# Kernel optimization log

Hardware: AMD Instinct MI355X
Metric: run time of the kernel (lower is better)

## Reference

```python
import jax, jax.numpy as jnp
import numpy as np

N_HEADS = 16

def setup_inputs() -> dict:
    key = jax.random.key(0)
    ks = jax.random.split(key, 5)
    D = 2048
    x = jax.random.normal(ks[0], (2, 2048, D), dtype=jnp.float32)
    scale = 1.0 / np.sqrt(D)
    Wq = jax.random.normal(ks[1], (D, D), dtype=jnp.float32) * scale
    Wk = jax.random.normal(ks[2], (D, D), dtype=jnp.float32) * scale
    Wv = jax.random.normal(ks[3], (D, D), dtype=jnp.float32) * scale
    Wo = jax.random.normal(ks[4], (D, D), dtype=jnp.float32) * scale
    return {"x": x, "Wq": Wq, "Wk": Wk, "Wv": Wv, "Wo": Wo}


def reference(x, Wq, Wk, Wv, Wo):
    # Causal multi-head attention. The original module computes it one query
    # position at a time (recompute loop) but the math is standard causal MHA:
    # query pos attends to key positions 0..pos.
    B, S, D = x.shape
    H = N_HEADS
    hd = D // H
    def split_heads(t):
        return t.reshape(B, S, H, hd).transpose(0, 2, 1, 3)  # (B,H,S,hd)
    q = split_heads(x @ Wq.T)
    k = split_heads(x @ Wk.T)
    v = split_heads(x @ Wv.T)
    scores = jnp.einsum('bhqd,bhkd->bhqk', q, k) / jnp.sqrt(jnp.asarray(hd, x.dtype))
    causal = jnp.tril(jnp.ones((S, S), dtype=bool))  # (S,S), True where allowed
    scores = jnp.where(causal[None, None], scores, jnp.asarray(-jnp.inf, scores.dtype))
    attn = jax.nn.softmax(scores, axis=-1)
    out = jnp.einsum('bhqk,bhkd->bhqd', attn, v)
    out = out.transpose(0, 2, 1, 3).reshape(B, S, D)
    return out @ Wo.T
```

## Files before the change

### kernel.cpp

```cpp
#include <hip/hip_runtime.h>
#include <stdint.h>

#define DD 2048
#define SS 2048
#define NB 2
#define NH 16
#define HDIM 128
#define MM (NB*SS)

typedef __attribute__((ext_vector_type(8))) short bf16x8;
typedef __attribute__((ext_vector_type(4))) float f32x4;
typedef __attribute__((ext_vector_type(4))) ushort u16x4;

__device__ __forceinline__ float fast_exp2(float x) {
  return __builtin_amdgcn_exp2f(x);
}

__device__ __forceinline__ ushort f2bf(float f) {
  union { float f; uint32_t u; } v; v.f = f;
  uint32_t u = v.u;
  return (ushort)((u + 0x7fffu + ((u >> 16) & 1u)) >> 16);
}

__device__ __forceinline__ void gld_lds16(const ushort* g, ushort* l) {
  __builtin_amdgcn_global_load_lds(
      (const __attribute__((address_space(1))) void*)g,
      (__attribute__((address_space(3))) void*)l, 16, 0, 0);
}

__global__ __launch_bounds__(256) void cvt_all(
    const float* __restrict__ x, const float* __restrict__ wq,
    const float* __restrict__ wk, const float* __restrict__ wv,
    const float* __restrict__ wo, ushort* __restrict__ dst)
{
  int i8 = blockIdx.x * 256 + threadIdx.x;
  const int X8 = MM * DD / 8;
  const int W8 = DD * DD / 8;
  const float* src; int off;
  if (i8 < X8)            { src = x;  off = i8; }
  else if (i8 < X8 +   W8){ src = wq; off = i8 - X8; }
  else if (i8 < X8 + 2*W8){ src = wk; off = i8 - (X8 +   W8); }
  else if (i8 < X8 + 3*W8){ src = wv; off = i8 - (X8 + 2*W8); }
  else                    { src = wo; off = i8 - (X8 + 3*W8); }
  const float4* p = (const float4*)src;
  float4 a = p[(long)off*2], b = p[(long)off*2 + 1];
  bf16x8 o;
  o[0]=(short)f2bf(a.x); o[1]=(short)f2bf(a.y); o[2]=(short)f2bf(a.z); o[3]=(short)f2bf(a.w);
  o[4]=(short)f2bf(b.x); o[5]=(short)f2bf(b.y); o[6]=(short)f2bf(b.z); o[7]=(short)f2bf(b.w);
  *(bf16x8*)(dst + (long)i8*8) = o;
}

template<int MODE>
__global__ __launch_bounds__(256, 2) void gemm_tri(
    const ushort* __restrict__ A, const ushort* __restrict__ Bt,
    ushort* __restrict__ Qo, ushort* __restrict__ Ko, ushort* __restrict__ Vt,
    float* __restrict__ Cf)
{
  __shared__ ushort lds[3 * 12288];
  const int t = threadIdx.x;
  const int bid = blockIdx.x;
  const int xcd = bid & 7, local = bid >> 3;
  const int NBX = (MODE == 0) ? 6 : 2;
  const int bm = local / NBX;
  const int bn = xcd * NBX + (local - bm * NBX);
  const int lane = t & 63, w = t >> 6;
  const int wr = w >> 1, wcn = w & 1;
  const int lr = lane & 15, lg = lane >> 4;

  int aoff[4], boff[2];
#pragma unroll
  for (int i = 0; i < 4; ++i) {
    int p = i*256 + t, ln = p >> 3, sr = (p & 7) ^ (ln & 7);
    aoff[i] = (2*ln + (sr >> 2)) * DD + (sr & 3) * 8;
  }
#pragma unroll
  for (int i = 0; i < 2; ++i) {
    int p = i*256 + t, ln = p >> 3, sr = (p & 7) ^ (ln & 7);
    boff[i] = (2*ln + (sr >> 2)) * DD + (sr & 3) * 8;
  }
  const ushort* Ab = A  + (long)(bm*256) * DD;
  const ushort* Bb = Bt + (long)(bn*128) * DD;

#define STG_A01(KT, BUF) do { const ushort* g_ = Ab + (KT)*32;             \
    ushort* l_ = lds + (BUF)*12288;                                        \
    gld_lds16(g_ + aoff[0], l_ + t*8);                                     \
    gld_lds16(g_ + aoff[1], l_ + (256 + t)*8); } while (0)
#define STG_A23(KT, BUF) do { const ushort* g_ = Ab + (KT)*32;             \
    ushort* l_ = lds + (BUF)*12288;                                        \
    gld_lds16(g_ + aoff[2], l_ + (512 + t)*8);                             \
    gld_lds16(g_ + aoff[3], l_ + (768 + t)*8); } while (0)
#define STG_B(KT, BUF)   do { const ushort* g_ = Bb + (KT)*32;             \
    ushort* l_ = lds + (BUF)*12288 + 8192;                                 \
    gld_lds16(g_ + boff[0], l_ + t*8);                                     \
    gld_lds16(g_ + boff[1], l_ + (256 + t)*8); } while (0)
#define LDA(dst, m) { int r_ = wr*128 + (m)*16 + lr; int ln_ = r_ >> 1;    \
    int sl_ = (lg + ((r_ & 1) << 2)) ^ (ln_ & 7);                          \
    (dst) = *(const bf16x8*)(cb + ln_*128 + sl_*16); }
#define LDB(dst, n) { int r_ = wcn*64 + (n)*16 + lr; int ln_ = r_ >> 1;    \
    int sl_ = (lg + ((r_ & 1) << 2)) ^ (ln_ & 7);                          \
    (dst) = *(const bf16x8*)(cb + 16384 + ln_*128 + sl_*16); }
#define MFMA42(AV, BV, MB, NB_) do {                                       \
    __builtin_amdgcn_s_setprio(1);                                         \
    _Pragma("unroll") for (int m = 0; m < 4; ++m)                          \
    _Pragma("unroll") for (int n = 0; n < 2; ++n)                          \
      acc[(MB)+m][(NB_)+n] = __builtin_amdgcn_mfma_f32_16x16x32_bf16(      \
          AV[m], BV[n], acc[(MB)+m][(NB_)+n], 0, 0, 0);                    \
    __builtin_amdgcn_s_setprio(0); } while (0)
#define SB  __builtin_amdgcn_sched_barrier(0)
#define BAR __builtin_amdgcn_s_barrier()
#define LGKM0 asm volatile("s_waitcnt lgkmcnt(0)" ::: "memory")

  f32x4 acc[8][4] = {};
  const int T = DD / 32;

  STG_A01(0, 0); STG_A23(0, 0); STG_B(0, 0);
  STG_A01(1, 1); STG_A23(1, 1); STG_B(1, 1);
  asm volatile("s_waitcnt vmcnt(6)" ::: "memory");
  SB; BAR; SB;

  for (int kt = 0; kt < T; ++kt) {
    const char* cb = (const char*)lds + (kt % 3) * 24576;
    const int bs = (kt + 2) % 3;
    const bool st = (kt + 2 < T);
    bf16x8 a03[4], a47[4], b01[2], b23[2];
    LDA(a03[0],0); LDA(a03[1],1); LDA(a03[2],2); LDA(a03[3],3);
    LDB(b01[0],0); LDB(b01[1],1);
    if (st) STG_A01(kt+2, bs);
    SB; BAR; LGKM0; SB;
    MFMA42(a03, b01, 0, 0);
    SB; BAR; SB;
    LDA(a47[0],4); LDA(a47[1],5); LDA(a47[2],6); LDA(a47[3],7);
    if (st) STG_A23(kt+2, bs);
    SB; BAR; LGKM0; SB;
    MFMA42(a47, b01, 4, 0);
    SB; BAR; SB;
    LDB(b23[0],2); LDB(b23[1],3);
    if (st) STG_B(kt+2, bs);
    SB; BAR; LGKM0; SB;
    MFMA42(a03, b23, 0, 2);
    SB; BAR; SB;
    if (st)              { asm volatile("s_waitcnt vmcnt(6)" ::: "memory"); }
    else if (kt + 1 < T) { asm volatile("s_waitcnt vmcnt(0)" ::: "memory"); }
    SB; BAR; SB;
    MFMA42(a47, b23, 4, 2);
    SB; BAR; SB;
  }
#undef STG_A01
#undef STG_A23
#undef STG_B
#undef LDA
#undef LDB
#undef MFMA42
#undef SB
#undef BAR
#undef LGKM0

  const int crb = bm*256 + wr*128 + lg*4;
  if (MODE == 0) {
    const int region = bn >> 4;
    const int ccb = (bn & 15)*128 + wcn*64 + lr;
    if (region < 2) {
      const float scale = (region == 0) ? (0.08838834764831845f * 1.4426950408889634f) : 1.0f;
      ushort* C = (region == 0) ? Qo : Ko;
#pragma unroll
      for (int m = 0; m < 8; ++m)
#pragma unroll
        for (int n = 0; n < 4; ++n)
#pragma unroll
          for (int j = 0; j < 4; ++j)
            C[(long)(crb + m*16 + j) * DD + (ccb + n*16)] = f2bf(acc[m][n][j] * scale);
    } else {
#pragma unroll
      for (int m = 0; m < 8; ++m) {
        int sg = crb + m*16;
        int b2 = sg >> 11, s2 = sg & 2047;
#pragma unroll
        for (int n = 0; n < 4; ++n) {
          int colv = ccb + n*16;
          int h2 = colv >> 7, d2 = colv & 127;
          u16x4 pk;
          pk[0] = f2bf(acc[m][n][0]); pk[1] = f2bf(acc[m][n][1]);
          pk[2] = f2bf(acc[m][n][2]); pk[3] = f2bf(acc[m][n][3]);
          *(u16x4*)(Vt + ((long)((b2*NH + h2)*HDIM + d2)) * SS + s2) = pk;
        }
      }
    }
  } else {
    const int ccb = bn*128 + wcn*64 + lr;
#pragma unroll
    for (int m = 0; m < 8; ++m)
#pragma unroll
      for (int n = 0; n < 4; ++n)
#pragma unroll
        for (int j = 0; j < 4; ++j)
          Cf[(long)(crb + m*16 + j) * DD + (ccb + n*16)] = acc[m][n][j];
  }
}

__global__ __launch_bounds__(512, 4) void attn_fwd(
    const ushort* __restrict__ Qb, const ushort* __restrict__ Kb,
    const ushort* __restrict__ Vtg, ushort* __restrict__ Ob)
{
  __shared__ ushort Ks[64*128];
  __shared__ ushort Vs[128*64];
  __shared__ ushort Ps[8*16*72];

  const int bid = blockIdx.x;
  const int qt = 15 - (bid >> 5);
  const int bh = bid & 31;
  const int b = bh >> 4, h = bh & 15;
  const int t = threadIdx.x;
  const int lane = t & 63;
  const int wq = t >> 6;
  const int lr = lane & 15, lg = lane >> 4;

  const int qbase = qt * 128;
  const long rowQ = (long)(b * SS + qbase + wq * 16);

  bf16x8 qf[4];
#pragma unroll
  for (int c = 0; c < 4; ++c)
    qf[c] = *(const bf16x8*)(Qb + (rowQ + lr) * DD + h*HDIM + c*32 + lg*8);

  f32x4 accO[8] = {};
  float mrow[4], lrow[4];
#pragma unroll
  for (int j = 0; j < 4; ++j) { mrow[j] = -1e30f; lrow[j] = 0.f; }

  const ushort* Kgb = Kb + (long)(b * SS) * DD + h * HDIM;
  const int kr0 = t >> 4, kr1 = 32 + (t >> 4), kci = t & 15;
  const ushort* gk0 = Kgb + (long)kr0 * DD + (kci ^ (kr0 & 7)) * 8;
  const ushort* gk1 = Kgb + (long)kr1 * DD + (kci ^ (kr1 & 7)) * 8;
  ushort* lk0 = Ks + t*8;
  ushort* lk1 = Ks + 4096 + t*8;

  const ushort* Vgb = Vtg + (long)(bh * HDIM) * SS;
  const int vd0 = t >> 3, vd1 = 64 + (t >> 3), vci = t & 7;
  const ushort* gv0 = Vgb + (long)vd0 * SS + (vci ^ (vd0 & 7)) * 8;
  const ushort* gv1 = Vgb + (long)vd1 * SS + (vci ^ (vd1 & 7)) * 8;
  ushort* lv0 = Vs + t*8;
  ushort* lv1 = Vs + 4096 + t*8;

  const int ktmax = 2*qt + 1;
  const int qminw = qbase + wq*16;
  const int qmaxw = qminw + 15;
  ushort* myP = Ps + wq * (16*72);

  for (int kt = 0; kt <= ktmax; ++kt) {
    const int k0 = kt * 64;
    gld_lds16(gk0, lk0); gld_lds16(gk1, lk1);
    gld_lds16(gv0, lv0); gld_lds16(gv1, lv1);
    gk0 += (long)64 * DD; gk1 += (long)64 * DD;
    gv0 += 64; gv1 += 64;
    __syncthreads();

    if (k0 <= qmaxw) {
      f32x4 sc[4] = {};
#pragma unroll
      for (int n = 0; n < 4; ++n) {
        int r = n*16 + lr;
        int swz = (r & 7) << 4;
#pragma unroll
        for (int c = 0; c < 4; ++c) {
          bf16x8 kf = *(const bf16x8*)((const char*)Ks + ((r*256 + c*64 + lg*16) ^ swz));
          sc[n] = __builtin_amdgcn_mfma_f32_16x16x32_bf16(qf[c], kf, sc[n], 0,0,0);
        }
      }
      if (k0 + 63 > qminw) {
#pragma unroll
        for (int n = 0; n < 4; ++n)
#pragma unroll
          for (int j = 0; j < 4; ++j) {
            int kpos = k0 + n*16 + lr;
            int qpos = qminw + lg*4 + j;
            if (kpos > qpos) sc[n][j] = -1e30f;
          }
      }
      float al[4];
#pragma unroll
      for (int j = 0; j < 4; ++j) {
        float tm = fmaxf(fmaxf(sc[0][j], sc[1][j]), fmaxf(sc[2][j], sc[3][j]));
#pragma unroll
        for (int off = 1; off < 16; off <<= 1) tm = fmaxf(tm, __shfl_xor(tm, off));
        float mn = fmaxf(mrow[j], tm);
        float a = fast_exp2(mrow[j] - mn);
        mrow[j] = mn;
        float ts = 0.f;
#pragma unroll
        for (int n = 0; n < 4; ++n) {
          float p = fast_exp2(sc[n][j] - mn);
          sc[n][j] = p; ts += p;
        }
#pragma unroll
        for (int off = 1; off < 16; off <<= 1) ts += __shfl_xor(ts, off);
        lrow[j] = lrow[j] * a + ts;
        al[j] = a;
      }
#pragma unroll
      for (int dg = 0; dg < 8; ++dg) {
        f32x4 v = accO[dg];
        v[0] *= al[0]; v[1] *= al[1]; v[2] *= al[2]; v[3] *= al[3];
        accO[dg] = v;
      }
#pragma unroll
      for (int n = 0; n < 4; ++n)
#pragma unroll
        for (int j = 0; j < 4; ++j)
          myP[(lg*4 + j)*72 + n*16 + lr] = f2bf(sc[n][j]);
      bf16x8 pa0 = *(const bf16x8*)(myP + lr*72 + lg*8);
      bf16x8 pa1 = *(const bf16x8*)(myP + lr*72 + 32 + lg*8);
#pragma unroll
      for (int dg = 0; dg < 8; ++dg) {
        int d = dg*16 + lr;
        int vswz = (d & 7) << 4;
        bf16x8 v0 = *(const bf16x8*)((const char*)Vs + ((d*128 + lg*16) ^ vswz));
        bf16x8 v1 = *(const bf16x8*)((const char*)Vs + ((d*128 + 64 + lg*16) ^ vswz));
        accO[dg] = __builtin_amdgcn_mfma_f32_16x16x32_bf16(pa0, v0, accO[dg], 0,0,0);
        accO[dg] = __builtin_amdgcn_mfma_f32_16x16x32_bf16(pa1, v1, accO[dg], 0,0,0);
      }
    }
    __syncthreads();
  }

  float inv[4];
#pragma unroll
  for (int j = 0; j < 4; ++j) inv[j] = 1.0f / lrow[j];
  ushort* Og = Ob + rowQ * DD + h * HDIM;
#pragma unroll
  for (int dg = 0; dg < 8; ++dg)
#pragma unroll
    for (int j = 0; j < 4; ++j)
      Og[(long)(lg*4 + j) * DD + dg*16 + lr] = f2bf(accO[dg][j] * inv[j]);
}

extern "C" void kernel_launch(void* const* d_in, const int* in_sizes, int n_in,
                              void* d_out, int out_size, void* d_ws, size_t ws_size,
                              hipStream_t stream) {
  const float* x  = (const float*)d_in[0];
  const float* Wq = (const float*)d_in[1];
  const float* Wk = (const float*)d_in[2];
  const float* Wv = (const float*)d_in[3];
  const float* Wo = (const float*)d_in[4];

  ushort* ws  = (ushort*)d_ws;
  ushort* xb  = ws;
  ushort* wqb = ws  + (long)MM*DD;
  ushort* wkb = wqb + (long)DD*DD;
  ushort* wvb = wkb + (long)DD*DD;
  ushort* wob = wvb + (long)DD*DD;
  ushort* Qb  = wob + (long)DD*DD;
  ushort* Kb  = Qb  + (long)MM*DD;
  ushort* Vtg = Kb  + (long)MM*DD;
  (void)wkb; (void)wvb;

  const int CVT_BLOCKS = (MM*DD + 4*DD*DD) / 8 / 256;
  cvt_all<<<CVT_BLOCKS, 256, 0, stream>>>(x, Wq, Wk, Wv, Wo, ws);

  gemm_tri<0><<<768, 256, 0, stream>>>(xb, wqb, Qb, Kb, Vtg, nullptr);

  attn_fwd<<<512, 512, 0, stream>>>(Qb, Kb, Vtg, xb);

  gemm_tri<1><<<256, 256, 0, stream>>>(xb, wob, nullptr, nullptr, nullptr,
                                       (float*)d_out);
}
```

Baseline: 274.8 us.

## Process 32 query rows per wave in attention to reuse K/V fragments

```diff
diff --git a/kernel.cpp b/kernel.cpp
--- a/kernel.cpp
+++ b/kernel.cpp
@@ -197,13 +197,13 @@
   }
 }
 
-__global__ __launch_bounds__(512, 4) void attn_fwd(
+__global__ __launch_bounds__(256, 3) void attn_fwd(
     const ushort* __restrict__ Qb, const ushort* __restrict__ Kb,
     const ushort* __restrict__ Vtg, ushort* __restrict__ Ob)
 {
   __shared__ ushort Ks[64*128];
   __shared__ ushort Vs[128*64];
-  __shared__ ushort Ps[8*16*72];
+  __shared__ ushort Ps[4*32*68];
 
   const int bid = blockIdx.x;
   const int qt = 15 - (bid >> 5);
@@ -215,47 +215,54 @@
   const int lr = lane & 15, lg = lane >> 4;
 
   const int qbase = qt * 128;
-  const long rowQ = (long)(b * SS + qbase + wq * 16);
-
-  bf16x8 qf[4];
-#pragma unroll
-  for (int c = 0; c < 4; ++c)
-    qf[c] = *(const bf16x8*)(Qb + (rowQ + lr) * DD + h*HDIM + c*32 + lg*8);
-
-  f32x4 accO[8] = {};
-  float mrow[4], lrow[4];
-#pragma unroll
-  for (int j = 0; j < 4; ++j) { mrow[j] = -1e30f; lrow[j] = 0.f; }
+  const long rowQ = (long)(b * SS + qbase + wq * 32);
+
+  bf16x8 qf[2][4];
+#pragma unroll
+  for (int i = 0; i < 2; ++i)
+#pragma unroll
+    for (int c = 0; c < 4; ++c)
+      qf[i][c] = *(const bf16x8*)(Qb + (rowQ + i*16 + lr) * DD + h*HDIM + c*32 + lg*8);
+
+  f32x4 accO[2][8] = {};
+  float mrow[2][4], lrow[2][4];
+#pragma unroll
+  for (int i = 0; i < 2; ++i)
+#pragma unroll
+    for (int j = 0; j < 4; ++j) { mrow[i][j] = -1e30f; lrow[i][j] = 0.f; }
 
   const ushort* Kgb = Kb + (long)(b * SS) * DD + h * HDIM;
-  const int kr0 = t >> 4, kr1 = 32 + (t >> 4), kci = t & 15;
-  const ushort* gk0 = Kgb + (long)kr0 * DD + (kci ^ (kr0 & 7)) * 8;
-  const ushort* gk1 = Kgb + (long)kr1 * DD + (kci ^ (kr1 & 7)) * 8;
-  ushort* lk0 = Ks + t*8;
-  ushort* lk1 = Ks + 4096 + t*8;
-
+  const ushort* gk[4]; ushort* lk[4];
+#pragma unroll
+  for (int i = 0; i < 4; ++i) {
+    int c = i*256 + t, kr = c >> 4, kc = c & 15;
+    gk[i] = Kgb + (long)kr * DD + (kc ^ (kr & 7)) * 8;
+    lk[i] = Ks + c*8;
+  }
   const ushort* Vgb = Vtg + (long)(bh * HDIM) * SS;
-  const int vd0 = t >> 3, vd1 = 64 + (t >> 3), vci = t & 7;
-  const ushort* gv0 = Vgb + (long)vd0 * SS + (vci ^ (vd0 & 7)) * 8;
-  const ushort* gv1 = Vgb + (long)vd1 * SS + (vci ^ (vd1 & 7)) * 8;
-  ushort* lv0 = Vs + t*8;
-  ushort* lv1 = Vs + 4096 + t*8;
+  const ushort* gv[4]; ushort* lv[4];
+#pragma unroll
+  for (int i = 0; i < 4; ++i) {
+    int c = i*256 + t, vd = c >> 3, vc = c & 7;
+    gv[i] = Vgb + (long)vd * SS + (vc ^ (vd & 7)) * 8;
+    lv[i] = Vs + c*8;
+  }
 
   const int ktmax = 2*qt + 1;
-  const int qminw = qbase + wq*16;
-  const int qmaxw = qminw + 15;
-  ushort* myP = Ps + wq * (16*72);
+  const int qminw = qbase + wq*32;
+  const int qmaxw = qminw + 31;
+  ushort* myP = Ps + wq * (32*68);
 
   for (int kt = 0; kt <= ktmax; ++kt) {
     const int k0 = kt * 64;
-    gld_lds16(gk0, lk0); gld_lds16(gk1, lk1);
-    gld_lds16(gv0, lv0); gld_lds16(gv1, lv1);
-    gk0 += (long)64 * DD; gk1 += (long)64 * DD;
-    gv0 += 64; gv1 += 64;
+#pragma unroll
+    for (int i = 0; i < 4; ++i) { gld_lds16(gk[i], lk[i]); gk[i] += (long)64 * DD; }
+#pragma unroll
+    for (int i = 0; i < 4; ++i) { gld_lds16(gv[i], lv[i]); gv[i] += 64; }
     __syncthreads();
 
     if (k0 <= qmaxw) {
-      f32x4 sc[4] = {};
+      f32x4 sc[2][4] = {};
 #pragma unroll
       for (int n = 0; n < 4; ++n) {
         int r = n*16 + lr;
@@ -263,74 +270,92 @@
 #pragma unroll
         for (int c = 0; c < 4; ++c) {
           bf16x8 kf = *(const bf16x8*)((const char*)Ks + ((r*256 + c*64 + lg*16) ^ swz));
-          sc[n] = __builtin_amdgcn_mfma_f32_16x16x32_bf16(qf[c], kf, sc[n], 0,0,0);
+          sc[0][n] = __builtin_amdgcn_mfma_f32_16x16x32_bf16(qf[0][c], kf, sc[0][n], 0,0,0);
+          sc[1][n] = __builtin_amdgcn_mfma_f32_16x16x32_bf16(qf[1][c], kf, sc[1][n], 0,0,0);
         }
       }
       if (k0 + 63 > qminw) {
 #pragma unroll
+        for (int i = 0; i < 2; ++i)
+#pragma unroll
+          for (int n = 0; n < 4; ++n)
+#pragma unroll
+            for (int j = 0; j < 4; ++j) {
+              int kpos = k0 + n*16 + lr;
+              int qpos = qminw + i*16 + lg*4 + j;
+              if (kpos > qpos) sc[i][n][j] = -1e30f;
+            }
+      }
+      float al[2][4];
+#pragma unroll
+      for (int i = 0; i < 2; ++i)
+#pragma unroll
+        for (int j = 0; j < 4; ++j) {
+          float tm = fmaxf(fmaxf(sc[i][0][j], sc[i][1][j]), fmaxf(sc[i][2][j], sc[i][3][j]));
+#pragma unroll
+          for (int off = 1; off < 16; off <<= 1) tm = fmaxf(tm, __shfl_xor(tm, off));
+          float mn = fmaxf(mrow[i][j], tm);
+          float a = fast_exp2(mrow[i][j] - mn);
+          mrow[i][j] = mn;
+          float ts = 0.f;
+#pragma unroll
+          for (int n = 0; n < 4; ++n) {
+            float p = fast_exp2(sc[i][n][j] - mn);
+            sc[i][n][j] = p; ts += p;
+          }
+#pragma unroll
+          for (int off = 1; off < 16; off <<= 1) ts += __shfl_xor(ts, off);
+          lrow[i][j] = lrow[i][j] * a + ts;
+          al[i][j] = a;
+        }
+#pragma unroll
+      for (int i = 0; i < 2; ++i)
+#pragma unroll
+        for (int dg = 0; dg < 8; ++dg) {
+          f32x4 v = accO[i][dg];
+          v[0] *= al[i][0]; v[1] *= al[i][1]; v[2] *= al[i][2]; v[3] *= al[i][3];
+          accO[i][dg] = v;
+        }
+#pragma unroll
+      for (int i = 0; i < 2; ++i)
+#pragma unroll
         for (int n = 0; n < 4; ++n)
 #pragma unroll
-          for (int j = 0; j < 4; ++j) {
-            int kpos = k0 + n*16 + lr;
-            int qpos = qminw + lg*4 + j;
-            if (kpos > qpos) sc[n][j] = -1e30f;
-          }
-      }
-      float al[4];
-#pragma unroll
-      for (int j = 0; j < 4; ++j) {
-        float tm = fmaxf(fmaxf(sc[0][j], sc[1][j]), fmaxf(sc[2][j], sc[3][j]));
-#pragma unroll
-        for (int off = 1; off < 16; off <<= 1) tm = fmaxf(tm, __shfl_xor(tm, off));
-        float mn = fmaxf(mrow[j], tm);
-        float a = fast_exp2(mrow[j] - mn);
-        mrow[j] = mn;
-        float ts = 0.f;
-#pragma unroll
-        for (int n = 0; n < 4; ++n) {
-          float p = fast_exp2(sc[n][j] - mn);
-          sc[n][j] = p; ts += p;
-        }
-#pragma unroll
-        for (int off = 1; off < 16; off <<= 1) ts += __shfl_xor(ts, off);
-        lrow[j] = lrow[j] * a + ts;
-        al[j] = a;
-      }
-#pragma unroll
-      for (int dg = 0; dg < 8; ++dg) {
-        f32x4 v = accO[dg];
-        v[0] *= al[0]; v[1] *= al[1]; v[2] *= al[2]; v[3] *= al[3];
-        accO[dg] = v;
-      }
-#pragma unroll
-      for (int n = 0; n < 4; ++n)
-#pragma unroll
-        for (int j = 0; j < 4; ++j)
-          myP[(lg*4 + j)*72 + n*16 + lr] = f2bf(sc[n][j]);
-      bf16x8 pa0 = *(const bf16x8*)(myP + lr*72 + lg*8);
-      bf16x8 pa1 = *(const bf16x8*)(myP + lr*72 + 32 + lg*8);
+          for (int j = 0; j < 4; ++j)
+            myP[(i*16 + lg*4 + j)*68 + n*16 + lr] = f2bf(sc[i][n][j]);
+      bf16x8 pa[2][2];
+#pragma unroll
+      for (int i = 0; i < 2; ++i)
+#pragma unroll
+        for (int kc = 0; kc < 2; ++kc)
+          pa[i][kc] = *(const bf16x8*)(myP + (i*16 + lr)*68 + kc*32 + lg*8);
 #pragma unroll
       for (int dg = 0; dg < 8; ++dg) {
         int d = dg*16 + lr;
         int vswz = (d & 7) << 4;
         bf16x8 v0 = *(const bf16x8*)((const char*)Vs + ((d*128 + lg*16) ^ vswz));
         bf16x8 v1 = *(const bf16x8*)((const char*)Vs + ((d*128 + 64 + lg*16) ^ vswz));
-        accO[dg] = __builtin_amdgcn_mfma_f32_16x16x32_bf16(pa0, v0, accO[dg], 0,0,0);
-        accO[dg] = __builtin_amdgcn_mfma_f32_16x16x32_bf16(pa1, v1, accO[dg], 0,0,0);
+        accO[0][dg] = __builtin_amdgcn_mfma_f32_16x16x32_bf16(pa[0][0], v0, accO[0][dg], 0,0,0);
+        accO[0][dg] = __builtin_amdgcn_mfma_f32_16x16x32_bf16(pa[0][1], v1, accO[0][dg], 0,0,0);
+        accO[1][dg] = __builtin_amdgcn_mfma_f32_16x16x32_bf16(pa[1][0], v0, accO[1][dg], 0,0,0);
+        accO[1][dg] = __builtin_amdgcn_mfma_f32_16x16x32_bf16(pa[1][1], v1, accO[1][dg], 0,0,0);
       }
     }
     __syncthreads();
   }
 
-  float inv[4];
-#pragma unroll
-  for (int j = 0; j < 4; ++j) inv[j] = 1.0f / lrow[j];
   ushort* Og = Ob + rowQ * DD + h * HDIM;
 #pragma unroll
-  for (int dg = 0; dg < 8; ++dg)
-#pragma unroll
-    for (int j = 0; j < 4; ++j)
-      Og[(long)(lg*4 + j) * DD + dg*16 + lr] = f2bf(accO[dg][j] * inv[j]);
+  for (int i = 0; i < 2; ++i) {
+    float inv[4];
+#pragma unroll
+    for (int j = 0; j < 4; ++j) inv[j] = 1.0f / lrow[i][j];
+#pragma unroll
+    for (int dg = 0; dg < 8; ++dg)
+#pragma unroll
+      for (int j = 0; j < 4; ++j)
+        Og[(long)(i*16 + lg*4 + j) * DD + dg*16 + lr] = f2bf(accO[i][dg][j] * inv[j]);
+  }
 }
 
 extern "C" void kernel_launch(void* const* d_in, const int* in_sizes, int n_in,
@@ -358,7 +383,7 @@
 
   gemm_tri<0><<<768, 256, 0, stream>>>(xb, wqb, Qb, Kb, Vtg, nullptr);
 
-  attn_fwd<<<512, 512, 0, stream>>>(Qb, Kb, Vtg, xb);
+  attn_fwd<<<512, 256, 0, stream>>>(Qb, Kb, Vtg, xb);
 
   gemm_tri<1><<<256, 256, 0, stream>>>(xb, wob, nullptr, nullptr, nullptr,
                                        (float*)d_out);
```

Measured after the change: 469.5 us. +70.8%, slower.

## Pair causal query tiles per block and double-buffer K/V loads

Applied to the files above, without the earlier changes.

```diff
diff --git a/kernel.cpp b/kernel.cpp
--- a/kernel.cpp
+++ b/kernel.cpp
@@ -201,12 +201,12 @@
     const ushort* __restrict__ Qb, const ushort* __restrict__ Kb,
     const ushort* __restrict__ Vtg, ushort* __restrict__ Ob)
 {
-  __shared__ ushort Ks[64*128];
-  __shared__ ushort Vs[128*64];
-  __shared__ ushort Ps[8*16*72];
+  __shared__ ushort Ks[2][64*128];
+  __shared__ ushort Vs[2][128*64];
+  __shared__ ushort Ps[8*16*68];
 
   const int bid = blockIdx.x;
-  const int qt = 15 - (bid >> 5);
+  const int p = bid >> 5;
   const int bh = bid & 31;
   const int b = bh >> 4, h = bh & 15;
   const int t = threadIdx.x;
@@ -214,123 +214,140 @@
   const int wq = t >> 6;
   const int lr = lane & 15, lg = lane >> 4;
 
-  const int qbase = qt * 128;
-  const long rowQ = (long)(b * SS + qbase + wq * 16);
-
-  bf16x8 qf[4];
-#pragma unroll
-  for (int c = 0; c < 4; ++c)
-    qf[c] = *(const bf16x8*)(Qb + (rowQ + lr) * DD + h*HDIM + c*32 + lg*8);
-
-  f32x4 accO[8] = {};
-  float mrow[4], lrow[4];
-#pragma unroll
-  for (int j = 0; j < 4; ++j) { mrow[j] = -1e30f; lrow[j] = 0.f; }
-
-  const ushort* Kgb = Kb + (long)(b * SS) * DD + h * HDIM;
-  const int kr0 = t >> 4, kr1 = 32 + (t >> 4), kci = t & 15;
-  const ushort* gk0 = Kgb + (long)kr0 * DD + (kci ^ (kr0 & 7)) * 8;
-  const ushort* gk1 = Kgb + (long)kr1 * DD + (kci ^ (kr1 & 7)) * 8;
-  ushort* lk0 = Ks + t*8;
-  ushort* lk1 = Ks + 4096 + t*8;
-
-  const ushort* Vgb = Vtg + (long)(bh * HDIM) * SS;
-  const int vd0 = t >> 3, vd1 = 64 + (t >> 3), vci = t & 7;
-  const ushort* gv0 = Vgb + (long)vd0 * SS + (vci ^ (vd0 & 7)) * 8;
-  const ushort* gv1 = Vgb + (long)vd1 * SS + (vci ^ (vd1 & 7)) * 8;
-  ushort* lv0 = Vs + t*8;
-  ushort* lv1 = Vs + 4096 + t*8;
-
-  const int ktmax = 2*qt + 1;
-  const int qminw = qbase + wq*16;
-  const int qmaxw = qminw + 15;
-  ushort* myP = Ps + wq * (16*72);
-
-  for (int kt = 0; kt <= ktmax; ++kt) {
-    const int k0 = kt * 64;
-    gld_lds16(gk0, lk0); gld_lds16(gk1, lk1);
-    gld_lds16(gv0, lv0); gld_lds16(gv1, lv1);
-    gk0 += (long)64 * DD; gk1 += (long)64 * DD;
-    gv0 += 64; gv1 += 64;
-    __syncthreads();
-
-    if (k0 <= qmaxw) {
-      f32x4 sc[4] = {};
-#pragma unroll
-      for (int n = 0; n < 4; ++n) {
-        int r = n*16 + lr;
-        int swz = (r & 7) << 4;
-#pragma unroll
-        for (int c = 0; c < 4; ++c) {
-          bf16x8 kf = *(const bf16x8*)((const char*)Ks + ((r*256 + c*64 + lg*16) ^ swz));
-          sc[n] = __builtin_amdgcn_mfma_f32_16x16x32_bf16(qf[c], kf, sc[n], 0,0,0);
-        }
+  int koff0, koff1, voff0, voff1;
+  { int c = t;       int kr = c >> 4, kc = c & 15; koff0 = kr*DD + ((kc ^ (kr & 7)) * 8); }
+  { int c = 512 + t; int kr = c >> 4, kc = c & 15; koff1 = kr*DD + ((kc ^ (kr & 7)) * 8); }
+  { int c = t;       int vd = c >> 3, vc = c & 7;  voff0 = vd*SS + ((vc ^ (vd & 7)) * 8); }
+  { int c = 512 + t; int vd = c >> 3, vc = c & 7;  voff1 = vd*SS + ((vc ^ (vd & 7)) * 8); }
+  const ushort* Kg = Kb + (long)(b * SS) * DD + h * HDIM;
+  const ushort* Vg = Vtg + (long)(bh * HDIM) * SS;
+
+#define STAGE(KT, BUF) do {                                   \
+    const ushort* kg_ = Kg + (long)(KT) * 64 * DD;            \
+    const ushort* vg_ = Vg + (KT) * 64;                       \
+    gld_lds16(kg_ + koff0, &Ks[BUF][t*8]);                    \
+    gld_lds16(kg_ + koff1, &Ks[BUF][4096 + t*8]);             \
+    gld_lds16(vg_ + voff0, &Vs[BUF][t*8]);                    \
+    gld_lds16(vg_ + voff1, &Vs[BUF][4096 + t*8]); } while (0)
+
+  ushort* myP = Ps + wq * (16*68);
+  int cur = 0;
+
+  STAGE(0, 0);
+  __syncthreads();
+
+  for (int half = 0; half < 2; ++half) {
+    const int qt = half ? (15 - p) : p;
+    const int qbase = qt * 128;
+    const long rowQ = (long)(b * SS + qbase + wq * 16);
+    const int ntile = 2*qt + 2;
+    const int qminw = qbase + wq*16;
+    const int qmaxw = qminw + 15;
+
+    bf16x8 qf[4];
+#pragma unroll
+    for (int c = 0; c < 4; ++c)
+      qf[c] = *(const bf16x8*)(Qb + (rowQ + lr) * DD + h*HDIM + c*32 + lg*8);
+
+    f32x4 accO[8] = {};
+    float mrow[4], lrow[4];
+#pragma unroll
+    for (int j = 0; j < 4; ++j) { mrow[j] = -1e30f; lrow[j] = 0.f; }
+
+    for (int kt = 0; kt < ntile; ++kt) {
+      const int k0 = kt * 64;
+      const bool last = (half == 1) && (kt == ntile - 1);
+      if (!last) {
+        const int ktn = (kt + 1 < ntile) ? (kt + 1) : 0;
+        STAGE(ktn, cur ^ 1);
       }
-      if (k0 + 63 > qminw) {
+
+      if (k0 <= qmaxw) {
+        const ushort* Kc = Ks[cur];
+        const ushort* Vc = Vs[cur];
+        f32x4 sc[4] = {};
+        __builtin_amdgcn_s_setprio(1);
+#pragma unroll
+        for (int n = 0; n < 4; ++n) {
+          int r = n*16 + lr;
+          int swz = (r & 7) << 4;
+#pragma unroll
+          for (int c = 0; c < 4; ++c) {
+            bf16x8 kf = *(const bf16x8*)((const char*)Kc + ((r*256 + c*64 + lg*16) ^ swz));
+            sc[n] = __builtin_amdgcn_mfma_f32_16x16x32_bf16(qf[c], kf, sc[n], 0,0,0);
+          }
+        }
+        __builtin_amdgcn_s_setprio(0);
+        if (k0 + 63 > qminw) {
+#pragma unroll
+          for (int n = 0; n < 4; ++n)
+#pragma unroll
+            for (int j = 0; j < 4; ++j) {
+              int kpos = k0 + n*16 + lr;
+              int qpos = qminw + lg*4 + j;
+              if (kpos > qpos) sc[n][j] = -1e30f;
+            }
+        }
+        float al[4];
+#pragma unroll
+        for (int j = 0; j < 4; ++j) {
+          float tm = fmaxf(fmaxf(sc[0][j], sc[1][j]), fmaxf(sc[2][j], sc[3][j]));
+#pragma unroll
+          for (int off = 1; off < 16; off <<= 1) tm = fmaxf(tm, __shfl_xor(tm, off));
+          float mn = fmaxf(mrow[j], tm);
+          float a = fast_exp2(mrow[j] - mn);
+          mrow[j] = mn;
+          float ts = 0.f;
+#pragma unroll
+          for (int n = 0; n < 4; ++n) {
+            float pv = fast_exp2(sc[n][j] - mn);
+            sc[n][j] = pv; ts += pv;
+          }
+#pragma unroll
+          for (int off = 1; off < 16; off <<= 1) ts += __shfl_xor(ts, off);
+          lrow[j] = lrow[j] * a + ts;
+          al[j] = a;
+        }
+#pragma unroll
+        for (int dg = 0; dg < 8; ++dg) {
+          f32x4 v = accO[dg];
+          v[0] *= al[0]; v[1] *= al[1]; v[2] *= al[2]; v[3] *= al[3];
+          accO[dg] = v;
+        }
 #pragma unroll
         for (int n = 0; n < 4; ++n)
 #pragma unroll
-          for (int j = 0; j < 4; ++j) {
-            int kpos = k0 + n*16 + lr;
-            int qpos = qminw + lg*4 + j;
-            if (kpos > qpos) sc[n][j] = -1e30f;
-          }
+          for (int j = 0; j < 4; ++j)
+            myP[(lg*4 + j)*68 + n*16 + lr] = f2bf(sc[n][j]);
+        bf16x8 pa0 = *(const bf16x8*)(myP + lr*68 + lg*8);
+        bf16x8 pa1 = *(const bf16x8*)(myP + lr*68 + 32 + lg*8);
+        __builtin_amdgcn_s_setprio(1);
+#pragma unroll
+        for (int dg = 0; dg < 8; ++dg) {
+          int d = dg*16 + lr;
+          int vswz = (d & 7) << 4;
+          bf16x8 v0 = *(const bf16x8*)((const char*)Vc + ((d*128 + lg*16) ^ vswz));
+          bf16x8 v1 = *(const bf16x8*)((const char*)Vc + ((d*128 + 64 + lg*16) ^ vswz));
+          accO[dg] = __builtin_amdgcn_mfma_f32_16x16x32_bf16(pa0, v0, accO[dg], 0,0,0);
+          accO[dg] = __builtin_amdgcn_mfma_f32_16x16x32_bf16(pa1, v1, accO[dg], 0,0,0);
+        }
+        __builtin_amdgcn_s_setprio(0);
       }
-      float al[4];
-#pragma unroll
-      for (int j = 0; j < 4; ++j) {
-        float tm = fmaxf(fmaxf(sc[0][j], sc[1][j]), fmaxf(sc[2][j], sc[3][j]));
-#pragma unroll
-        for (int off = 1; off < 16; off <<= 1) tm = fmaxf(tm, __shfl_xor(tm, off));
-        float mn = fmaxf(mrow[j], tm);
-        float a = fast_exp2(mrow[j] - mn);
-        mrow[j] = mn;
-        float ts = 0.f;
-#pragma unroll
-        for (int n = 0; n < 4; ++n) {
-          float p = fast_exp2(sc[n][j] - mn);
-          sc[n][j] = p; ts += p;
-        }
-#pragma unroll
-        for (int off = 1; off < 16; off <<= 1) ts += __shfl_xor(ts, off);
-        lrow[j] = lrow[j] * a + ts;
-        al[j] = a;
-      }
-#pragma unroll
-      for (int dg = 0; dg < 8; ++dg) {
-        f32x4 v = accO[dg];
-        v[0] *= al[0]; v[1] *= al[1]; v[2] *= al[2]; v[3] *= al[3];
-        accO[dg] = v;
-      }
-#pragma unroll
-      for (int n = 0; n < 4; ++n)
-#pragma unroll
-        for (int j = 0; j < 4; ++j)
-          myP[(lg*4 + j)*72 + n*16 + lr] = f2bf(sc[n][j]);
-      bf16x8 pa0 = *(const bf16x8*)(myP + lr*72 + lg*8);
-      bf16x8 pa1 = *(const bf16x8*)(myP + lr*72 + 32 + lg*8);
-#pragma unroll
-      for (int dg = 0; dg < 8; ++dg) {
-        int d = dg*16 + lr;
-        int vswz = (d & 7) << 4;
-        bf16x8 v0 = *(const bf16x8*)((const char*)Vs + ((d*128 + lg*16) ^ vswz));
-        bf16x8 v1 = *(const bf16x8*)((const char*)Vs + ((d*128 + 64 + lg*16) ^ vswz));
-        accO[dg] = __builtin_amdgcn_mfma_f32_16x16x32_bf16(pa0, v0, accO[dg], 0,0,0);
-        accO[dg] = __builtin_amdgcn_mfma_f32_16x16x32_bf16(pa1, v1, accO[dg], 0,0,0);
-      }
+      __syncthreads();
+      cur ^= 1;
     }
-    __syncthreads();
-  }
-
-  float inv[4];
-#pragma unroll
-  for (int j = 0; j < 4; ++j) inv[j] = 1.0f / lrow[j];
-  ushort* Og = Ob + rowQ * DD + h * HDIM;
-#pragma unroll
-  for (int dg = 0; dg < 8; ++dg)
-#pragma unroll
-    for (int j = 0; j < 4; ++j)
-      Og[(long)(lg*4 + j) * DD + dg*16 + lr] = f2bf(accO[dg][j] * inv[j]);
+
+    float inv[4];
+#pragma unroll
+    for (int j = 0; j < 4; ++j) inv[j] = 1.0f / lrow[j];
+    ushort* Og = Ob + rowQ * DD + h * HDIM;
+#pragma unroll
+    for (int dg = 0; dg < 8; ++dg)
+#pragma unroll
+      for (int j = 0; j < 4; ++j)
+        Og[(long)(lg*4 + j) * DD + dg*16 + lr] = f2bf(accO[dg][j] * inv[j]);
+  }
+#undef STAGE
 }
 
 extern "C" void kernel_launch(void* const* d_in, const int* in_sizes, int n_in,
@@ -358,7 +375,7 @@
 
   gemm_tri<0><<<768, 256, 0, stream>>>(xb, wqb, Qb, Kb, Vtg, nullptr);
 
-  attn_fwd<<<512, 512, 0, stream>>>(Qb, Kb, Vtg, xb);
+  attn_fwd<<<256, 512, 0, stream>>>(Qb, Kb, Vtg, xb);
 
   gemm_tri<1><<<256, 256, 0, stream>>>(xb, wob, nullptr, nullptr, nullptr,
                                        (float*)d_out);
```

Result: faster. 264.4 us (-3.8%).
